# Performance work log

Measured on AMD Instinct MI355X. Metric: run time of the kernel, lower is better.

Reference implementation:

```python
import jax, jax.numpy as jnp
import numpy as np

NUM_SITES = 64
PHYS_DIM = 2
BOND_DIM = 32
BATCH = 65536


def _build_mps(num_sites, phys_dim, bond_dim, seed=0):
    """Replicates ImprovedMPS._initialize_tensors + _canonical_form, then
    zero-pads ragged cores into a dense [S, D, p, D] stack."""
    rng = np.random.default_rng(seed)
    tensors = []
    cur = 1
    for i in range(num_sites):
        if i == 0:
            nb = min(bond_dim, phys_dim)
            shape = (1, phys_dim, nb)
            cur = nb
        elif i == num_sites - 1:
            shape = (cur, phys_dim, 1)
        else:
            nb = min(bond_dim, cur * phys_dim)
            shape = (cur, phys_dim, nb)
            cur = nb
        ld, rd = shape[0] * shape[1], shape[2]
        m = (rng.standard_normal((ld, rd)) * 0.1).astype(np.float32)
        if ld >= rd:
            q, _ = np.linalg.qr(m)
            t = q.reshape(shape)
        else:
            q, _ = np.linalg.qr(m.T)
            t = q.T.reshape(shape)
        tensors.append(t.astype(np.float32))
    # left-canonical sweep
    for i in range(num_sites - 1):
        l, p, r = tensors[i].shape
        q, rr = np.linalg.qr(tensors[i].reshape(l * p, r))
        tensors[i] = q.reshape(l, p, q.shape[1]).astype(np.float32)
        nl, npd, nr = tensors[i + 1].shape
        tensors[i + 1] = (rr @ tensors[i + 1].reshape(nl, npd * nr)).reshape(rr.shape[0], npd, nr).astype(np.float32)
    # zero-pad ragged bonds into dense stack [S, D, p, D]
    A = np.zeros((num_sites, bond_dim, phys_dim, bond_dim), dtype=np.float32)
    for i, t in enumerate(tensors):
        l, p, r = t.shape
        A[i, :l, :, :r] = t
    return A


def setup_inputs() -> dict:
    key = jax.random.key(0)
    x_batch = jax.random.normal(key, (BATCH, NUM_SITES, PHYS_DIM), dtype=jnp.float32)
    A = jnp.asarray(_build_mps(NUM_SITES, PHYS_DIM, BOND_DIM))
    return {"x_batch": x_batch, "A": A}


def reference(x_batch, A):
    # x_batch: [B, S, p]; A: [S, D, p, D] (zero-padded ragged MPS cores)
    B = x_batch.shape[0]
    D = A.shape[1]
    # left_vector starts as ones(B,1) in the ragged view == one-hot e0 in padded view
    left0 = jnp.zeros((B, D), dtype=x_batch.dtype).at[:, 0].set(1.0)
    xs = jnp.moveaxis(x_batch, 1, 0)  # [S, B, p]

    def step(left, inp):
        A_i, x_i = inp  # [D, p, D], [B, p]
        # fuses: contracted = einsum('bp,lpd->bld'); left = einsum('bl,bld->bd')
        left = jnp.einsum('bl,bp,lpd->bd', left, x_i, A_i)
        return left, None

    left, _ = jax.lax.scan(step, left0, (A, xs))
    return left[:, :1]  # last core has right bond 1 -> only col 0 is nonzero
```

## Files before the change

kernel.cpp:

```cpp
#include <hip/hip_runtime.h>


typedef _Float16 half8 __attribute__((ext_vector_type(8)));
typedef float floatx16 __attribute__((ext_vector_type(16)));
typedef float f32x4 __attribute__((ext_vector_type(4)));

#define NSITES 64
#define CHUNK_ELEMS 16384

__global__ void mps_prep_afrag(const float* __restrict__ A, _Float16* __restrict__ Af) {
    __shared__ float sA[2048];
    const int site = blockIdx.x;
    const int tid  = threadIdx.x;
#pragma unroll
    for (int i = 0; i < 8; ++i) sA[tid + 256 * i] = A[site * 2048 + tid + 256 * i];
    __syncthreads();
    const int f    = tid >> 6;
    const int lane = tid & 63;
    const int h    = lane >> 5;
    const int d    = lane & 31;
    half8 v;
#pragma unroll
    for (int e = 0; e < 8; ++e) {
        int kg = f * 16 + h * 8 + e;
        v[e] = (_Float16)sA[((kg >> 1) * 2 + (kg & 1)) * 32 + d];
    }
    reinterpret_cast<half8*>(Af)[(site * 4 + f) * 64 + lane] = v;
}

#define FRAG(BF, ACC, F, X0, X1)                                              \
    {                                                                         \
        float c0_ = ACC[4 * (F) + 0], c1_ = ACC[4 * (F) + 1];                 \
        float c2_ = ACC[4 * (F) + 2], c3_ = ACC[4 * (F) + 3];                 \
        BF[0] = (_Float16)(c0_ * (X0)); BF[1] = (_Float16)(c0_ * (X1));       \
        BF[2] = (_Float16)(c1_ * (X0)); BF[3] = (_Float16)(c1_ * (X1));       \
        BF[4] = (_Float16)(c2_ * (X0)); BF[5] = (_Float16)(c2_ * (X1));       \
        BF[6] = (_Float16)(c3_ * (X0)); BF[7] = (_Float16)(c3_ * (X1));       \
    }

#define STEP(SL, AIN, AOUT, XB, J)                                            \
    {                                                                         \
        const float x0_ = XB[2 * (J)], x1_ = XB[2 * (J) + 1];                 \
        half8 b0_, b1_, b2_, b3_;                                             \
        FRAG(b0_, AIN, 0, x0_, x1_);                                          \
        FRAG(b1_, AIN, 1, x0_, x1_);                                          \
        FRAG(b2_, AIN, 2, x0_, x1_);                                          \
        FRAG(b3_, AIN, 3, x0_, x1_);                                          \
        floatx16 t0_ = __builtin_amdgcn_mfma_f32_32x32x16_f16(SL[0], b0_, zv, 0, 0, 0); \
        floatx16 t1_ = __builtin_amdgcn_mfma_f32_32x32x16_f16(SL[2], b2_, zv, 0, 0, 0); \
        t0_ = __builtin_amdgcn_mfma_f32_32x32x16_f16(SL[1], b1_, t0_, 0, 0, 0);         \
        t1_ = __builtin_amdgcn_mfma_f32_32x32x16_f16(SL[3], b3_, t1_, 0, 0, 0);         \
        AOUT = t0_ + t1_;                                                     \
    }

#define RDFRAG(DST, BUF, S)                                                   \
    {                                                                         \
        _Pragma("unroll")                                                     \
        for (int f_ = 0; f_ < 4; ++f_)                                        \
            DST[f_] = *(const half8*)&smA[BUF][(((S) * 4 + f_) * 64 + lane) * 8]; \
    }

#define STAGE(C, BUF)                                                         \
    {                                                                         \
        _Pragma("unroll")                                                     \
        for (int r_ = 0; r_ < 4; ++r_) {                                      \
            const int rec_ = r_ * 8 + wid;                                    \
            const _Float16* g_ = Af + (size_t)(C) * CHUNK_ELEMS + rec_ * 512 + lane * 8; \
            __builtin_amdgcn_global_load_lds(                                 \
                (const __attribute__((address_space(1))) void*)g_,            \
                (__attribute__((address_space(3))) void*)&smA[BUF][rec_ * 512], \
                16, 0, 0);                                                    \
        }                                                                     \
    }

#define LOADX(DST, OCT)                                                       \
    {                                                                         \
        f32x4 t0_ = xp[(OCT) * 4 + 0];                                        \
        f32x4 t1_ = xp[(OCT) * 4 + 1];                                        \
        f32x4 t2_ = xp[(OCT) * 4 + 2];                                        \
        f32x4 t3_ = xp[(OCT) * 4 + 3];                                        \
        DST[0]  = t0_[0]; DST[1]  = t0_[1]; DST[2]  = t0_[2]; DST[3]  = t0_[3]; \
        DST[4]  = t1_[0]; DST[5]  = t1_[1]; DST[6]  = t1_[2]; DST[7]  = t1_[3]; \
        DST[8]  = t2_[0]; DST[9]  = t2_[1]; DST[10] = t2_[2]; DST[11] = t2_[3]; \
        DST[12] = t3_[0]; DST[13] = t3_[1]; DST[14] = t3_[2]; DST[15] = t3_[3]; \
    }

#define CHUNK_BODY(C, BUF, SBUF, XCUR, XNEXT, DO_STAGE, DO_NEXT)              \
    {                                                                         \
        if (DO_STAGE) STAGE((C) + 2, SBUF);                                   \
        if (DO_NEXT) LOADX(XNEXT, (C) + 1);                                   \
        STEP(F0, acc, nacc, XCUR, 0) RDFRAG(F0, BUF, 2)                       \
        STEP(F1, nacc, acc, XCUR, 1) RDFRAG(F1, BUF, 3)                       \
        STEP(F0, acc, nacc, XCUR, 2) RDFRAG(F0, BUF, 4)                       \
        STEP(F1, nacc, acc, XCUR, 3) RDFRAG(F1, BUF, 5)                       \
        STEP(F0, acc, nacc, XCUR, 4) RDFRAG(F0, BUF, 6)                       \
        STEP(F1, nacc, acc, XCUR, 5) RDFRAG(F1, BUF, 7)                       \
        STEP(F0, acc, nacc, XCUR, 6)                                          \
        STEP(F1, nacc, acc, XCUR, 7)                                          \
        __syncthreads();                                                      \
        if (DO_NEXT) { RDFRAG(F0, ((C) + 1) % 3, 0) RDFRAG(F1, ((C) + 1) % 3, 1) } \
    }

__global__ __launch_bounds__(512) void mps_main(const float* __restrict__ x,
                                                const _Float16* __restrict__ Af,
                                                float* __restrict__ out) {
    __shared__ __align__(16) _Float16 smA[3][CHUNK_ELEMS];

    const int lane = threadIdx.x & 63;
    const int wid  = threadIdx.x >> 6;
    const int row0 = (blockIdx.x * 8 + wid) * 32;
    const int col  = lane & 31;
    const int b    = row0 + col;

    const f32x4* xp = reinterpret_cast<const f32x4*>(x + (size_t)b * (NSITES * 2));

    floatx16 zv;
#pragma unroll
    for (int i = 0; i < 16; ++i) zv[i] = 0.f;

    floatx16 acc, nacc;
#pragma unroll
    for (int i = 0; i < 16; ++i) { acc[i] = 0.f; nacc[i] = 0.f; }
    if (lane < 32) acc[0] = 1.f;

    float xa[16], xb[16];
    half8 F0[4], F1[4];

    STAGE(0, 0);
    STAGE(1, 1);
    LOADX(xa, 0);
    __syncthreads();
    RDFRAG(F0, 0, 0)
    RDFRAG(F1, 0, 1)

    CHUNK_BODY(0,  0,  2,    xa,  xb,   1,    1)
    CHUNK_BODY(1,  1,  0,    xb,  xa,   1,    1)
    CHUNK_BODY(2,  2,  1,    xa,  xb,   1,    1)
    CHUNK_BODY(3,  0,  2,    xb,  xa,   1,    1)
    CHUNK_BODY(4,  1,  0,    xa,  xb,   1,    1)
    CHUNK_BODY(5,  2,  1,    xb,  xa,   1,    1)
    CHUNK_BODY(6,  0,  2,    xa,  xb,   0,    1)
    CHUNK_BODY(7,  1,  0,    xb,  xa,   0,    0)

    if (lane < 32) out[row0 + lane] = acc[0];
}

extern "C" void kernel_launch(void* const* d_in, const int* in_sizes, int n_in,
                              void* d_out, int out_size, void* d_ws, size_t ws_size,
                              hipStream_t stream) {
    const float* x = (const float*)d_in[0];
    const float* A = (const float*)d_in[1];
    float* outp = (float*)d_out;
    _Float16* Af = (_Float16*)d_ws;

    hipLaunchKernelGGL(mps_prep_afrag, dim3(NSITES), dim3(256), 0, stream, A, Af);
    hipLaunchKernelGGL(mps_main, dim3(65536 / 256), dim3(512), 0, stream, x, Af, outp);
}
```

Measured before the change: 35.45 us.

## Switch to 16x16x32 MFMA with 16 rows per wave and double buffering

Replaces the 32x32x16 MFMA chain with 16x16x32 MFMAs, so each wave handles 16 batch rows, and doubles the grid to 512 blocks. The A-fragment prep layout is rewritten to match the new operand layout. LDS staging drops from triple to double buffering, and launch bounds now request 4 blocks per CU for higher occupancy and more parallelism. The trade-off is that each wave's dependent MFMA chain does less work, and loads are staged only one chunk ahead, which gives less prefetch slack.

```diff
diff --git a/kernel.cpp b/kernel.cpp
--- a/kernel.cpp
+++ b/kernel.cpp
@@ -2,7 +2,7 @@
 
 
 typedef _Float16 half8 __attribute__((ext_vector_type(8)));
-typedef float floatx16 __attribute__((ext_vector_type(16)));
+typedef float floatx4 __attribute__((ext_vector_type(4)));
 typedef float f32x4 __attribute__((ext_vector_type(4)));
 
 #define NSITES 64
@@ -15,42 +15,36 @@
 #pragma unroll
     for (int i = 0; i < 8; ++i) sA[tid + 256 * i] = A[site * 2048 + tid + 256 * i];
     __syncthreads();
-    const int f    = tid >> 6;
-    const int lane = tid & 63;
-    const int h    = lane >> 5;
-    const int d    = lane & 31;
+    const int f     = tid >> 6;
+    const int lane  = tid & 63;
+    const int d     = 16 * (f >> 1) + (lane & 15);
+    const int kbase = 32 * (f & 1) + (lane >> 4) * 8;
     half8 v;
 #pragma unroll
-    for (int e = 0; e < 8; ++e) {
-        int kg = f * 16 + h * 8 + e;
-        v[e] = (_Float16)sA[((kg >> 1) * 2 + (kg & 1)) * 32 + d];
-    }
+    for (int e = 0; e < 8; ++e)
+        v[e] = (_Float16)sA[(kbase + e) * 32 + d];
     reinterpret_cast<half8*>(Af)[(site * 4 + f) * 64 + lane] = v;
 }
 
-#define FRAG(BF, ACC, F, X0, X1)                                              \
+#define FRAGU(U, AC, X0, X1)                                                  \
     {                                                                         \
-        float c0_ = ACC[4 * (F) + 0], c1_ = ACC[4 * (F) + 1];                 \
-        float c2_ = ACC[4 * (F) + 2], c3_ = ACC[4 * (F) + 3];                 \
-        BF[0] = (_Float16)(c0_ * (X0)); BF[1] = (_Float16)(c0_ * (X1));       \
-        BF[2] = (_Float16)(c1_ * (X0)); BF[3] = (_Float16)(c1_ * (X1));       \
-        BF[4] = (_Float16)(c2_ * (X0)); BF[5] = (_Float16)(c2_ * (X1));       \
-        BF[6] = (_Float16)(c3_ * (X0)); BF[7] = (_Float16)(c3_ * (X1));       \
+        float c0_ = AC[0], c1_ = AC[1], c2_ = AC[2], c3_ = AC[3];             \
+        U[0] = (_Float16)(c0_ * (X0)); U[1] = (_Float16)(c0_ * (X1));         \
+        U[2] = (_Float16)(c1_ * (X0)); U[3] = (_Float16)(c1_ * (X1));         \
+        U[4] = (_Float16)(c2_ * (X0)); U[5] = (_Float16)(c2_ * (X1));         \
+        U[6] = (_Float16)(c3_ * (X0)); U[7] = (_Float16)(c3_ * (X1));         \
     }
 
-#define STEP(SL, AIN, AOUT, XB, J)                                            \
+#define STEP(SL, AI0, AI1, AO0, AO1, XB, J)                                   \
     {                                                                         \
         const float x0_ = XB[2 * (J)], x1_ = XB[2 * (J) + 1];                 \
-        half8 b0_, b1_, b2_, b3_;                                             \
-        FRAG(b0_, AIN, 0, x0_, x1_);                                          \
-        FRAG(b1_, AIN, 1, x0_, x1_);                                          \
-        FRAG(b2_, AIN, 2, x0_, x1_);                                          \
-        FRAG(b3_, AIN, 3, x0_, x1_);                                          \
-        floatx16 t0_ = __builtin_amdgcn_mfma_f32_32x32x16_f16(SL[0], b0_, zv, 0, 0, 0); \
-        floatx16 t1_ = __builtin_amdgcn_mfma_f32_32x32x16_f16(SL[2], b2_, zv, 0, 0, 0); \
-        t0_ = __builtin_amdgcn_mfma_f32_32x32x16_f16(SL[1], b1_, t0_, 0, 0, 0);         \
-        t1_ = __builtin_amdgcn_mfma_f32_32x32x16_f16(SL[3], b3_, t1_, 0, 0, 0);         \
-        AOUT = t0_ + t1_;                                                     \
+        half8 u0_, u1_;                                                       \
+        FRAGU(u0_, AI0, x0_, x1_);                                            \
+        FRAGU(u1_, AI1, x0_, x1_);                                            \
+        AO0 = __builtin_amdgcn_mfma_f32_16x16x32_f16(SL[0], u0_, zv, 0, 0, 0);   \
+        AO1 = __builtin_amdgcn_mfma_f32_16x16x32_f16(SL[2], u0_, zv, 0, 0, 0);   \
+        AO0 = __builtin_amdgcn_mfma_f32_16x16x32_f16(SL[1], u1_, AO0, 0, 0, 0);  \
+        AO1 = __builtin_amdgcn_mfma_f32_16x16x32_f16(SL[3], u1_, AO1, 0, 0, 0);  \
     }
 
 #define RDFRAG(DST, BUF, S)                                                   \
@@ -85,64 +79,61 @@
         DST[12] = t3_[0]; DST[13] = t3_[1]; DST[14] = t3_[2]; DST[15] = t3_[3]; \
     }
 
-#define CHUNK_BODY(C, BUF, SBUF, XCUR, XNEXT, DO_STAGE, DO_NEXT)              \
+#define CHUNK_BODY(C, BUF, XCUR, XNEXT, DO_NEXT)                              \
     {                                                                         \
-        if (DO_STAGE) STAGE((C) + 2, SBUF);                                   \
-        if (DO_NEXT) LOADX(XNEXT, (C) + 1);                                   \
-        STEP(F0, acc, nacc, XCUR, 0) RDFRAG(F0, BUF, 2)                       \
-        STEP(F1, nacc, acc, XCUR, 1) RDFRAG(F1, BUF, 3)                       \
-        STEP(F0, acc, nacc, XCUR, 2) RDFRAG(F0, BUF, 4)                       \
-        STEP(F1, nacc, acc, XCUR, 3) RDFRAG(F1, BUF, 5)                       \
-        STEP(F0, acc, nacc, XCUR, 4) RDFRAG(F0, BUF, 6)                       \
-        STEP(F1, nacc, acc, XCUR, 5) RDFRAG(F1, BUF, 7)                       \
-        STEP(F0, acc, nacc, XCUR, 6)                                          \
-        STEP(F1, nacc, acc, XCUR, 7)                                          \
+        if (DO_NEXT) { STAGE((C) + 1, 1 - (BUF)); LOADX(XNEXT, (C) + 1); }    \
+        STEP(F0, a0, a1, n0, n1, XCUR, 0) RDFRAG(F0, BUF, 2)                  \
+        STEP(F1, n0, n1, a0, a1, XCUR, 1) RDFRAG(F1, BUF, 3)                  \
+        STEP(F0, a0, a1, n0, n1, XCUR, 2) RDFRAG(F0, BUF, 4)                  \
+        STEP(F1, n0, n1, a0, a1, XCUR, 3) RDFRAG(F1, BUF, 5)                  \
+        STEP(F0, a0, a1, n0, n1, XCUR, 4) RDFRAG(F0, BUF, 6)                  \
+        STEP(F1, n0, n1, a0, a1, XCUR, 5) RDFRAG(F1, BUF, 7)                  \
+        STEP(F0, a0, a1, n0, n1, XCUR, 6)                                     \
+        STEP(F1, n0, n1, a0, a1, XCUR, 7)                                     \
         __syncthreads();                                                      \
-        if (DO_NEXT) { RDFRAG(F0, ((C) + 1) % 3, 0) RDFRAG(F1, ((C) + 1) % 3, 1) } \
+        if (DO_NEXT) { RDFRAG(F0, 1 - (BUF), 0) RDFRAG(F1, 1 - (BUF), 1) }    \
     }
 
-__global__ __launch_bounds__(512) void mps_main(const float* __restrict__ x,
-                                                const _Float16* __restrict__ Af,
-                                                float* __restrict__ out) {
-    __shared__ __align__(16) _Float16 smA[3][CHUNK_ELEMS];
+__global__ __launch_bounds__(512, 4) void mps_main(const float* __restrict__ x,
+                                                   const _Float16* __restrict__ Af,
+                                                   float* __restrict__ out) {
+    __shared__ __align__(16) _Float16 smA[2][CHUNK_ELEMS];
 
     const int lane = threadIdx.x & 63;
     const int wid  = threadIdx.x >> 6;
-    const int row0 = (blockIdx.x * 8 + wid) * 32;
-    const int col  = lane & 31;
-    const int b    = row0 + col;
+    const int row0 = (blockIdx.x * 8 + wid) * 16;
+    const int b    = row0 + (lane & 15);
 
     const f32x4* xp = reinterpret_cast<const f32x4*>(x + (size_t)b * (NSITES * 2));
 
-    floatx16 zv;
+    floatx4 zv;
 #pragma unroll
-    for (int i = 0; i < 16; ++i) zv[i] = 0.f;
+    for (int i = 0; i < 4; ++i) zv[i] = 0.f;
 
-    floatx16 acc, nacc;
+    floatx4 a0, a1, n0, n1;
 #pragma unroll
-    for (int i = 0; i < 16; ++i) { acc[i] = 0.f; nacc[i] = 0.f; }
-    if (lane < 32) acc[0] = 1.f;
+    for (int i = 0; i < 4; ++i) { a0[i] = 0.f; a1[i] = 0.f; n0[i] = 0.f; n1[i] = 0.f; }
+    if (lane < 16) a0[0] = 1.f;
 
-    float xa[16], xb[16];
+    float xa[16], xb2[16];
     half8 F0[4], F1[4];
 
     STAGE(0, 0);
-    STAGE(1, 1);
     LOADX(xa, 0);
     __syncthreads();
     RDFRAG(F0, 0, 0)
     RDFRAG(F1, 0, 1)
 
-    CHUNK_BODY(0,  0,  2,    xa,  xb,   1,    1)
-    CHUNK_BODY(1,  1,  0,    xb,  xa,   1,    1)
-    CHUNK_BODY(2,  2,  1,    xa,  xb,   1,    1)
-    CHUNK_BODY(3,  0,  2,    xb,  xa,   1,    1)
-    CHUNK_BODY(4,  1,  0,    xa,  xb,   1,    1)
-    CHUNK_BODY(5,  2,  1,    xb,  xa,   1,    1)
-    CHUNK_BODY(6,  0,  2,    xa,  xb,   0,    1)
-    CHUNK_BODY(7,  1,  0,    xb,  xa,   0,    0)
+    CHUNK_BODY(0, 0, xa,  xb2, 1)
+    CHUNK_BODY(1, 1, xb2, xa,  1)
+    CHUNK_BODY(2, 0, xa,  xb2, 1)
+    CHUNK_BODY(3, 1, xb2, xa,  1)
+    CHUNK_BODY(4, 0, xa,  xb2, 1)
+    CHUNK_BODY(5, 1, xb2, xa,  1)
+    CHUNK_BODY(6, 0, xa,  xb2, 1)
+    CHUNK_BODY(7, 1, xb2, xa,  0)
 
-    if (lane < 32) out[row0 + lane] = acc[0];
+    if (lane < 16) out[row0 + lane] = a0[0];
 }
 
 extern "C" void kernel_launch(void* const* d_in, const int* in_sizes, int n_in,
@@ -154,5 +145,5 @@
     _Float16* Af = (_Float16*)d_ws;
 
     hipLaunchKernelGGL(mps_prep_afrag, dim3(NSITES), dim3(256), 0, stream, A, Af);
-    hipLaunchKernelGGL(mps_main, dim3(65536 / 256), dim3(512), 0, stream, x, Af, outp);
+    hipLaunchKernelGGL(mps_main, dim3(65536 / 128), dim3(512), 0, stream, x, Af, outp);
 }
```

Measured after the change: 35.78 us. No clear change (+0.9%).
